# Kernel tuning notes

Hardware: AMD Instinct MI355X
Metric: run time of the kernel (lower is better)

## Reference

```python
import jax, jax.numpy as jnp
import numpy as np

# Synthetic production-scale triangle mesh: dense HxW grid.
H = 512
W = 512
V = H * W           # num_vertices = 262144
B = 32              # batch of meshes


def _grid_faces(h, w):
    # Two triangles per quad cell; vertex (i,j) -> index i*w + j.
    i, j = np.meshgrid(np.arange(h - 1), np.arange(w - 1), indexing='ij')
    v = (i * w + j).ravel()
    f1 = np.stack([v, v + 1, v + w], axis=1)
    f2 = np.stack([v + 1, v + w + 1, v + w], axis=1)
    return np.concatenate([f1, f2], axis=0).astype(np.int64)  # (F, 3)


def _laplacian_edges(faces, num_vertices):
    # Unique undirected edges from the 3 sides of every triangle.
    e = np.concatenate([faces[:, [0, 1]], faces[:, [1, 2]], faces[:, [2, 0]]], axis=0)
    e = np.sort(e, axis=1)
    e = np.unique(e, axis=0)                      # (E_und, 2)
    rows = np.concatenate([e[:, 0], e[:, 1]])     # directed: both orientations
    cols = np.concatenate([e[:, 1], e[:, 0]])
    deg = np.bincount(rows, minlength=num_vertices).astype(np.float32)
    vals = -1.0 / deg[rows]                       # row-normalized off-diagonal of L
    return rows.astype(np.int32), cols.astype(np.int32), vals.astype(np.float32)


def setup_inputs() -> dict:
    key = jax.random.key(0)
    faces = _grid_faces(H, W)
    rows, cols, vals = _laplacian_edges(faces, V)
    vertices = jax.random.normal(key, (B, V, 3), dtype=jnp.float32)
    return {
        'vertices': vertices,
        'rows': jnp.asarray(rows),   # (2E,) int32 — destination vertex of each Laplacian entry
        'cols': jnp.asarray(cols),   # (2E,) int32 — source   vertex of each Laplacian entry
        'vals': jnp.asarray(vals),   # (2E,) float32 — -1/deg[row]
    }


def reference(vertices, rows, cols, vals):
    # L @ v == v + scatter_add(vals * v[cols]) : identity diagonal + normalized neighbors.
    num_v = vertices.shape[1]
    gathered = vertices[:, cols, :] * vals[None, :, None]        # (B, 2E, 3)
    neigh = jax.vmap(lambda g: jax.ops.segment_sum(g, rows, num_segments=num_v))(gathered)
    Lv = vertices + neigh                                        # (B, V, 3)
    # torch: (Lv ** 2).sum(dim=-1).mean()  -> mean over (B, V) of squared norms
    return jnp.mean(jnp.sum(Lv * Lv, axis=-1))
```

## Files before the change

kernel.cpp:

```cpp
#include <hip/hip_runtime.h>


#define GH 512
#define GW 512
#define GV (GH * GW)
#define NBLK 4096

__global__ __launch_bounds__(256) void lap_partial_kernel(
    const float* __restrict__ verts, float* __restrict__ partials, int B) {
    const long long total = (long long)B * GV;
    const long long nthreads = (long long)gridDim.x * blockDim.x;
    const long long tid0 = (long long)blockIdx.x * blockDim.x + threadIdx.x;

    float local = 0.0f;
    for (long long idx = tid0; idx < total; idx += nthreads) {
        const int b = (int)(idx >> 18);
        const int v = (int)(idx & (GV - 1));
        const int i = v >> 9;
        const int j = v & (GW - 1);
        const float* __restrict__ base = verts + (long long)b * GV * 3;

        float sx = 0.f, sy = 0.f, sz = 0.f;
        int deg = 0;

        #define ACC(vv) { const float* p = base + (long long)(vv) * 3; \
                          sx += p[0]; sy += p[1]; sz += p[2]; deg++; }
        if (j > 0)                  ACC(v - 1);
        if (j < GW - 1)             ACC(v + 1);
        if (i > 0)                  ACC(v - GW);
        if (i < GH - 1)             ACC(v + GW);
        if (i > 0 && j < GW - 1)    ACC(v - GW + 1);
        if (i < GH - 1 && j > 0)    ACC(v + GW - 1);
        #undef ACC

        const float inv = -1.0f / (float)deg;
        const float* p = base + (long long)v * 3;
        const float lx = fmaf(inv, sx, p[0]);
        const float ly = fmaf(inv, sy, p[1]);
        const float lz = fmaf(inv, sz, p[2]);
        local += lx * lx + ly * ly + lz * lz;
    }

    #pragma unroll
    for (int off = 32; off > 0; off >>= 1)
        local += __shfl_down(local, off, 64);

    __shared__ float wsum[4];
    const int lane = threadIdx.x & 63;
    const int wid  = threadIdx.x >> 6;
    if (lane == 0) wsum[wid] = local;
    __syncthreads();

    if (threadIdx.x == 0)
        partials[blockIdx.x] = wsum[0] + wsum[1] + wsum[2] + wsum[3];
}

__global__ __launch_bounds__(256) void lap_final_kernel(
    const float* __restrict__ partials, float* __restrict__ out, int nblk, int B) {
    float local = 0.0f;
    for (int k = threadIdx.x; k < nblk; k += 256)
        local += partials[k];

    #pragma unroll
    for (int off = 32; off > 0; off >>= 1)
        local += __shfl_down(local, off, 64);

    __shared__ float wsum[4];
    const int lane = threadIdx.x & 63;
    const int wid  = threadIdx.x >> 6;
    if (lane == 0) wsum[wid] = local;
    __syncthreads();

    if (threadIdx.x == 0) {
        const float s = wsum[0] + wsum[1] + wsum[2] + wsum[3];
        out[0] = s / ((float)B * (float)GV);
    }
}

extern "C" void kernel_launch(void* const* d_in, const int* in_sizes, int n_in,
                              void* d_out, int out_size, void* d_ws, size_t ws_size,
                              hipStream_t stream) {
    const float* verts = (const float*)d_in[0];
    float* out = (float*)d_out;
    float* partials = (float*)d_ws;

    const int B = in_sizes[0] / (GV * 3);

    lap_partial_kernel<<<NBLK, 256, 0, stream>>>(verts, partials, B);
    lap_final_kernel<<<1, 256, 0, stream>>>(partials, out, NBLK, B);
}
```

Before: 191.3 us.

## Stream grid rows per block with register sliding window and float4 loads

Replaces the per-vertex gather of six neighbours with a row-streaming stencil. Each block owns a 16-row strip of one batch mesh, and each thread loads one float4 of a row. Horizontal neighbours come from wave shuffles plus halo loads at the wave edges, and vertical contributions are carried in registers across iterations. This removes the redundant scattered neighbour reads and uses coalesced vector loads, at the cost of re-reading two halo rows per strip. NBLK and the grid are now fixed to 32 batches, so the kernel no longer handles other batch sizes.

```diff
diff --git a/kernel.cpp b/kernel.cpp
--- a/kernel.cpp
+++ b/kernel.cpp
@@ -4,55 +4,117 @@
 #define GH 512
 #define GW 512
 #define GV (GH * GW)
-#define NBLK 4096
+#define ROWF 1536
+#define RQ 384
+#define RI 16
+#define NCHUNK (GH / RI)
+#define NITER (RI + 2)
+#define NBLK (32 * NCHUNK)
 
-__global__ __launch_bounds__(256) void lap_partial_kernel(
-    const float* __restrict__ verts, float* __restrict__ partials, int B) {
-    const long long total = (long long)B * GV;
-    const long long nthreads = (long long)gridDim.x * blockDim.x;
-    const long long tid0 = (long long)blockIdx.x * blockDim.x + threadIdx.x;
+__global__ __launch_bounds__(RQ, 6) void lap_partial_kernel(
+    const float* __restrict__ verts, float* __restrict__ partials) {
+    const int bid   = blockIdx.x;
+    const int batch = bid >> 5;
+    const int chunk = bid & 31;
+    const int i0    = chunk * RI;
+    const int t     = threadIdx.x;
+    const int lane  = t & 63;
+    const float* __restrict__ base = verts + (size_t)batch * (GV * 3) + 4 * t;
 
-    float local = 0.0f;
-    for (long long idx = tid0; idx < total; idx += nthreads) {
-        const int b = (int)(idx >> 18);
-        const int v = (int)(idx & (GV - 1));
-        const int i = v >> 9;
-        const int j = v & (GW - 1);
-        const float* __restrict__ base = verts + (long long)b * GV * 3;
+    float invM[4], invT[4], invB[4];
+    #pragma unroll
+    for (int e = 0; e < 4; ++e) {
+        const int q = 4 * t + e;
+        const float jl = (q >= 3) ? 1.f : 0.f;
+        const float jr = (q < ROWF - 3) ? 1.f : 0.f;
+        invM[e] = -1.f / (2.f + 2.f * jl + 2.f * jr);
+        invT[e] = -1.f / (1.f + 2.f * jl + jr);
+        invB[e] = -1.f / (1.f + jl + 2.f * jr);
+    }
+    const bool needHL = (lane == 0)  && (t > 0);
+    const bool needHR = (lane == 63) && (t < RQ - 1);
 
-        float sx = 0.f, sy = 0.f, sz = 0.f;
-        int deg = 0;
+    float4 qn = make_float4(0.f, 0.f, 0.f, 0.f);
+    float nhl0 = 0, nhl1 = 0, nhl2 = 0, nhr0 = 0, nhr1 = 0, nhr2 = 0;
+    if (i0 > 0) {
+        const float* rp = base + (size_t)(i0 - 1) * ROWF;
+        qn = *(const float4*)rp;
+        if (needHL) { nhl0 = rp[-3]; nhl1 = rp[-2]; nhl2 = rp[-1]; }
+        if (needHR) { nhr0 = rp[4];  nhr1 = rp[5];  nhr2 = rp[6]; }
+    }
 
-        #define ACC(vv) { const float* p = base + (long long)(vv) * 3; \
-                          sx += p[0]; sy += p[1]; sz += p[2]; deg++; }
-        if (j > 0)                  ACC(v - 1);
-        if (j < GW - 1)             ACC(v + 1);
-        if (i > 0)                  ACC(v - GW);
-        if (i < GH - 1)             ACC(v + GW);
-        if (i > 0 && j < GW - 1)    ACC(v - GW + 1);
-        if (i < GH - 1 && j > 0)    ACC(v + GW - 1);
-        #undef ACC
+    float4 T2 = make_float4(0,0,0,0), T1 = T2, M1 = T2, C1 = T2;
+    float local = 0.f;
 
-        const float inv = -1.0f / (float)deg;
-        const float* p = base + (long long)v * 3;
-        const float lx = fmaf(inv, sx, p[0]);
-        const float ly = fmaf(inv, sy, p[1]);
-        const float lz = fmaf(inv, sz, p[2]);
-        local += lx * lx + ly * ly + lz * lz;
+    #pragma unroll 2
+    for (int k = 0; k < NITER; ++k) {
+        const float4 Q = qn;
+        const float chl0 = nhl0, chl1 = nhl1, chl2 = nhl2;
+        const float chr0 = nhr0, chr1 = nhr1, chr2 = nhr2;
+
+        nhl0 = 0; nhl1 = 0; nhl2 = 0; nhr0 = 0; nhr1 = 0; nhr2 = 0;
+        const int rn = i0 + k;
+        if (k < NITER - 1 && rn < GH) {
+            const float* rp = base + (size_t)rn * ROWF;
+            qn = *(const float4*)rp;
+            if (needHL) { nhl0 = rp[-3]; nhl1 = rp[-2]; nhl2 = rp[-1]; }
+            if (needHR) { nhr0 = rp[4];  nhr1 = rp[5];  nhr2 = rp[6]; }
+        } else {
+            qn = make_float4(0.f, 0.f, 0.f, 0.f);
+        }
+
+        const float py = __shfl_up(Q.y, 1, 64);
+        const float pz = __shfl_up(Q.z, 1, 64);
+        const float pw = __shfl_up(Q.w, 1, 64);
+        const float nx = __shfl_down(Q.x, 1, 64);
+        const float ny = __shfl_down(Q.y, 1, 64);
+        const float nz = __shfl_down(Q.z, 1, 64);
+
+        float4 Qm3, Qp3;
+        Qm3.x = (lane == 0)  ? chl0 : py;
+        Qm3.y = (lane == 0)  ? chl1 : pz;
+        Qm3.z = (lane == 0)  ? chl2 : pw;
+        Qm3.w = Q.x;
+        Qp3.x = Q.w;
+        Qp3.y = (lane == 63) ? chr0 : nx;
+        Qp3.z = (lane == 63) ? chr1 : ny;
+        Qp3.w = (lane == 63) ? chr2 : nz;
+
+        float4 Bn, Tn, Mn;
+        Bn.x = Q.x + Qm3.x; Bn.y = Q.y + Qm3.y; Bn.z = Q.z + Qm3.z; Bn.w = Q.w + Qm3.w;
+        Tn.x = Q.x + Qp3.x; Tn.y = Q.y + Qp3.y; Tn.z = Q.z + Qp3.z; Tn.w = Q.w + Qp3.w;
+        Mn.x = Qm3.x + Qp3.x; Mn.y = Qm3.y + Qp3.y; Mn.z = Qm3.z + Qp3.z; Mn.w = Qm3.w + Qp3.w;
+
+        if (k >= 2) {
+            const int c = i0 + k - 2;
+            const float* inv = invM;
+            if (c == 0) inv = invT;
+            else if (c == GH - 1) inv = invB;
+
+            float s, lv;
+            s = T2.x + M1.x + Bn.x; lv = fmaf(inv[0], s, C1.x); local = fmaf(lv, lv, local);
+            s = T2.y + M1.y + Bn.y; lv = fmaf(inv[1], s, C1.y); local = fmaf(lv, lv, local);
+            s = T2.z + M1.z + Bn.z; lv = fmaf(inv[2], s, C1.z); local = fmaf(lv, lv, local);
+            s = T2.w + M1.w + Bn.w; lv = fmaf(inv[3], s, C1.w); local = fmaf(lv, lv, local);
+        }
+
+        T2 = T1; T1 = Tn; M1 = Mn; C1 = Q;
     }
 
     #pragma unroll
     for (int off = 32; off > 0; off >>= 1)
         local += __shfl_down(local, off, 64);
 
-    __shared__ float wsum[4];
-    const int lane = threadIdx.x & 63;
-    const int wid  = threadIdx.x >> 6;
-    if (lane == 0) wsum[wid] = local;
+    __shared__ float wsum[6];
+    const int wave = t >> 6;
+    if (lane == 0) wsum[wave] = local;
     __syncthreads();
-
-    if (threadIdx.x == 0)
-        partials[blockIdx.x] = wsum[0] + wsum[1] + wsum[2] + wsum[3];
+    if (t == 0) {
+        float s = wsum[0];
+        #pragma unroll
+        for (int w = 1; w < 6; ++w) s += wsum[w];
+        partials[bid] = s;
+    }
 }
 
 __global__ __launch_bounds__(256) void lap_final_kernel(
@@ -86,6 +148,6 @@
 
     const int B = in_sizes[0] / (GV * 3);
 
-    lap_partial_kernel<<<NBLK, 256, 0, stream>>>(verts, partials, B);
+    lap_partial_kernel<<<NBLK, RQ, 0, stream>>>(verts, partials);
     lap_final_kernel<<<1, 256, 0, stream>>>(partials, out, NBLK, B);
 }
```

New measurement: 165.1 us. 13.7% less time.
